# Kernel optimization log

Measured on AMD Instinct MI355X. Metric: run time of the kernel, lower is better.

The kernel has to match this reference:

```python
import jax, jax.numpy as jnp
import numpy as np

DIM = 1024
B, T = 4, 8192


def setup_inputs() -> dict:
    key = jax.random.key(0)
    ks = jax.random.split(key, 5)
    scale = 1.0 / np.sqrt(DIM)
    x = jax.random.normal(ks[0], (B, T, DIM), dtype=jnp.float32)
    w_in = jax.random.uniform(ks[1], (DIM, DIM), jnp.float32, -scale, scale)
    b_in = jax.random.uniform(ks[2], (DIM,), jnp.float32, -scale, scale)
    a = jnp.zeros((DIM,), jnp.float32)   # nn.Parameter(torch.zeros(dim))
    b = jnp.ones((DIM,), jnp.float32)    # nn.Parameter(torch.ones(dim))
    w_out = jax.random.uniform(ks[3], (DIM, DIM), jnp.float32, -scale, scale)
    b_out = jax.random.uniform(ks[4], (DIM,), jnp.float32, -scale, scale)
    return {"x": x, "w_in": w_in, "b_in": b_in, "a": a, "b": b,
            "w_out": w_out, "b_out": b_out}


def reference(x, w_in, b_in, a, b, w_out, b_out):
    # h = in_proj(x): [B, T, D]
    h = jnp.einsum('btd,ed->bte', x, w_in) + b_in
    A = jax.nn.sigmoid(a)  # [D], diagonal transition

    def step(state, h_t):
        state = A * state + b * h_t  # [B, D]
        return state, state

    init = jnp.zeros_like(h[:, 0])  # [B, D]
    _, ys = jax.lax.scan(step, init, jnp.swapaxes(h, 0, 1))  # ys: [T, B, D]
    y = jnp.swapaxes(ys, 0, 1)  # [B, T, D]
    return jnp.einsum('btd,ed->bte', y, w_out) + b_out
```

## Files before the change

### kernel.cpp

```cpp
#include <hip/hip_runtime.h>
#include <hip/hip_bf16.h>
#include <cstdint>

#define DIM 1024
#define BATCH 4
#define SEQ 8192
#define M_TOTAL (BATCH * SEQ)

#define CH 64
#define CL (SEQ / CH)

using bf16 = __hip_bfloat16;
typedef __attribute__((ext_vector_type(4))) float f32x4;
typedef __attribute__((ext_vector_type(8))) __bf16 bf16x8;

__global__ void f32_to_bf16_vec(const float* __restrict__ in,
                                bf16* __restrict__ out, long n4) {
    long i = blockIdx.x * (long)blockDim.x + threadIdx.x;
    if (i >= n4) return;
    const float4 v = ((const float4*)in)[i];
    __hip_bfloat162* o = (__hip_bfloat162*)(out + i * 4);
    o[0] = __float22bfloat162_rn(make_float2(v.x, v.y));
    o[1] = __float22bfloat162_rn(make_float2(v.z, v.w));
}

template <int OUT_MODE>
__global__ __launch_bounds__(256) void gemm_bt_kernel(
    const bf16* __restrict__ A, const bf16* __restrict__ B,
    const float* __restrict__ bias, void* __restrict__ C,
    int M, int N, int K) {
    __shared__ __align__(16) char lds[2 * 128 * 32 * 2];
    char* ldsA = lds;
    char* ldsB = lds + 128 * 32 * 2;

    const int tid  = threadIdx.x;
    const int wave = tid >> 6;
    const int lane = tid & 63;
    const int bm = blockIdx.x;
    const int bn = blockIdx.y;
    const int wm = (wave >> 1) * 64;
    const int wn = (wave & 1) * 64;

    f32x4 acc[4][4];
#pragma unroll
    for (int i = 0; i < 4; i++)
#pragma unroll
        for (int j = 0; j < 4; j++) acc[i][j] = (f32x4){0.f, 0.f, 0.f, 0.f};

    const long arow_base = (long)bm * 128;
    const long brow_base = (long)bn * 128;

    const int fr_row = lane & 15;
    const int fr_kb  = lane >> 4;

    for (int k0 = 0; k0 < K; k0 += 32) {
#pragma unroll
        for (int r = 0; r < 2; r++) {
            int c = tid + r * 256;
            int row = c >> 2, kc = c & 3;
            const bf16* ga = A + (arow_base + row) * K + k0 + kc * 8;
            const bf16* gb = B + (brow_base + row) * K + k0 + kc * 8;
            __builtin_amdgcn_global_load_lds(
                (const __attribute__((address_space(1))) void*)ga,
                (__attribute__((address_space(3))) void*)(ldsA + c * 16),
                16, 0, 0);
            __builtin_amdgcn_global_load_lds(
                (const __attribute__((address_space(1))) void*)gb,
                (__attribute__((address_space(3))) void*)(ldsB + c * 16),
                16, 0, 0);
        }
        __syncthreads();

        bf16x8 af[4], bfg[4];
#pragma unroll
        for (int i = 0; i < 4; i++) {
            int rowA = wm + i * 16 + fr_row;
            af[i] = *(const bf16x8*)(ldsA + rowA * 64 + fr_kb * 16);
        }
#pragma unroll
        for (int j = 0; j < 4; j++) {
            int rowB = wn + j * 16 + fr_row;
            bfg[j] = *(const bf16x8*)(ldsB + rowB * 64 + fr_kb * 16);
        }
#pragma unroll
        for (int i = 0; i < 4; i++)
#pragma unroll
            for (int j = 0; j < 4; j++)
                acc[i][j] = __builtin_amdgcn_mfma_f32_16x16x32_bf16(
                    af[i], bfg[j], acc[i][j], 0, 0, 0);
        __syncthreads();
    }

    const int crow = (lane >> 4) * 4;
    const int ccol = lane & 15;
#pragma unroll
    for (int i = 0; i < 4; i++) {
#pragma unroll
        for (int j = 0; j < 4; j++) {
            long mbase = (long)bm * 128 + wm + i * 16 + crow;
            int n = bn * 128 + wn + j * 16 + ccol;
            float bv = bias[n];
#pragma unroll
            for (int r = 0; r < 4; r++) {
                float v = acc[i][j][r] + bv;
                long idx = (mbase + r) * (long)N + n;
                if (OUT_MODE == 0)
                    ((bf16*)C)[idx] = __float2bfloat16(v);
                else
                    ((float*)C)[idx] = v;
            }
        }
    }
}

__global__ __launch_bounds__(1024) void scan_pass1(
    const bf16* __restrict__ h, const float* __restrict__ a,
    const float* __restrict__ bcoef, float* __restrict__ S) {
    const int d = threadIdx.x;
    const int blk = blockIdx.x;
    const int b = blk / CH, c = blk % CH;
    const float Ad = 1.f / (1.f + expf(-a[d]));
    const float bd = bcoef[d];
    float s = 0.f;
    const bf16* hp = h + ((long)b * SEQ + (long)c * CL) * DIM + d;
#pragma unroll 4
    for (int t = 0; t < CL; t++)
        s = Ad * s + bd * __bfloat162float(hp[(long)t * DIM]);
    S[((long)b * CH + c) * DIM + d] = s;
}

__global__ __launch_bounds__(1024) void scan_pass2(
    const float* __restrict__ S, const float* __restrict__ a,
    float* __restrict__ In) {
    const int d = threadIdx.x;
    const int b = blockIdx.x;
    const float Ad = 1.f / (1.f + expf(-a[d]));
    float Ap = Ad;
#pragma unroll
    for (int i = 0; i < 7; i++) Ap *= Ap;
    float carry = 0.f;
    for (int c = 0; c < CH; c++) {
        In[((long)b * CH + c) * DIM + d] = carry;
        carry = Ap * carry + S[((long)b * CH + c) * DIM + d];
    }
}

__global__ __launch_bounds__(1024) void scan_pass3(
    bf16* __restrict__ h, const float* __restrict__ a,
    const float* __restrict__ bcoef, const float* __restrict__ In) {
    const int d = threadIdx.x;
    const int blk = blockIdx.x;
    const int b = blk / CH, c = blk % CH;
    const float Ad = 1.f / (1.f + expf(-a[d]));
    const float bd = bcoef[d];
    float s = In[((long)b * CH + c) * DIM + d];
    bf16* hp = h + ((long)b * SEQ + (long)c * CL) * DIM + d;
#pragma unroll 4
    for (int t = 0; t < CL; t++) {
        s = Ad * s + bd * __bfloat162float(hp[(long)t * DIM]);
        hp[(long)t * DIM] = __float2bfloat16(s);
    }
}

extern "C" void kernel_launch(void* const* d_in, const int* in_sizes, int n_in,
                              void* d_out, int out_size, void* d_ws,
                              size_t ws_size, hipStream_t stream) {
    const float* x     = (const float*)d_in[0];
    const float* w_in  = (const float*)d_in[1];
    const float* b_in  = (const float*)d_in[2];
    const float* a     = (const float*)d_in[3];
    const float* bcoef = (const float*)d_in[4];
    const float* w_out = (const float*)d_in[5];
    const float* b_out = (const float*)d_in[6];
    float* out = (float*)d_out;

    char* ws = (char*)d_ws;
    bf16* xb  = (bf16*)ws;  ws += (size_t)M_TOTAL * DIM * 2;
    bf16* wib = (bf16*)ws;  ws += (size_t)DIM * DIM * 2;
    bf16* wob = (bf16*)ws;  ws += (size_t)DIM * DIM * 2;
    bf16* h   = (bf16*)ws;  ws += (size_t)M_TOTAL * DIM * 2;
    float* S  = (float*)ws; ws += (size_t)BATCH * CH * DIM * 4;
    float* In = (float*)ws; ws += (size_t)BATCH * CH * DIM * 4;

    {
        long n4 = (long)M_TOTAL * DIM / 4;
        f32_to_bf16_vec<<<(int)((n4 + 255) / 256), 256, 0, stream>>>(x, xb, n4);
        long w4 = (long)DIM * DIM / 4;
        f32_to_bf16_vec<<<(int)((w4 + 255) / 256), 256, 0, stream>>>(w_in, wib, w4);
        f32_to_bf16_vec<<<(int)((w4 + 255) / 256), 256, 0, stream>>>(w_out, wob, w4);
    }

    dim3 gg(M_TOTAL / 128, DIM / 128);

    gemm_bt_kernel<0><<<gg, 256, 0, stream>>>(xb, wib, b_in, h, M_TOTAL, DIM, DIM);

    scan_pass1<<<BATCH * CH, DIM, 0, stream>>>(h, a, bcoef, S);
    scan_pass2<<<BATCH, DIM, 0, stream>>>(S, a, In);
    scan_pass3<<<BATCH * CH, DIM, 0, stream>>>(h, a, bcoef, In);

    gemm_bt_kernel<1><<<gg, 256, 0, stream>>>(h, wob, b_out, out, M_TOTAL, DIM, DIM);
}
```

Before: 467.1 us.

## Fuse conversion kernels, widen GEMM K-tile with swizzled LDS, fold scan carry pass

Merges the three fp32-to-bf16 conversion launches into one kernel. The GEMM K-tile grows from 32 to 64 and uses an XOR-swizzled LDS layout to cut bank conflicts and halve the number of barriers per K. The grid is transposed so consecutive blocks share the same A rows. The separate carry-propagation scan pass is removed: each chunk block recomputes its incoming carry from the chunk sums, and the scan unroll factor is raised. This adds redundant per-block carry work and doubles LDS per block, which may lower occupancy.

Measured after the change: 448.8 us. -3.9%, faster.

```diff
diff --git a/kernel.cpp b/kernel.cpp
--- a/kernel.cpp
+++ b/kernel.cpp
@@ -14,12 +14,20 @@
 typedef __attribute__((ext_vector_type(4))) float f32x4;
 typedef __attribute__((ext_vector_type(8))) __bf16 bf16x8;
 
-__global__ void f32_to_bf16_vec(const float* __restrict__ in,
-                                bf16* __restrict__ out, long n4) {
+__global__ void convert_all(const float* __restrict__ x, bf16* __restrict__ xb,
+                            const float* __restrict__ w1, bf16* __restrict__ w1b,
+                            const float* __restrict__ w2, bf16* __restrict__ w2b,
+                            long n4x, long n4w) {
     long i = blockIdx.x * (long)blockDim.x + threadIdx.x;
-    if (i >= n4) return;
-    const float4 v = ((const float4*)in)[i];
-    __hip_bfloat162* o = (__hip_bfloat162*)(out + i * 4);
+    const float* in;
+    bf16* out;
+    long off;
+    if (i < n4x)              { in = x;  out = xb;  off = i; }
+    else if (i < n4x + n4w)   { in = w1; out = w1b; off = i - n4x; }
+    else if (i < n4x + 2*n4w) { in = w2; out = w2b; off = i - n4x - n4w; }
+    else return;
+    const float4 v = ((const float4*)in)[off];
+    __hip_bfloat162* o = (__hip_bfloat162*)(out + off * 4);
     o[0] = __float22bfloat162_rn(make_float2(v.x, v.y));
     o[1] = __float22bfloat162_rn(make_float2(v.z, v.w));
 }
@@ -29,15 +37,15 @@
     const bf16* __restrict__ A, const bf16* __restrict__ B,
     const float* __restrict__ bias, void* __restrict__ C,
     int M, int N, int K) {
-    __shared__ __align__(16) char lds[2 * 128 * 32 * 2];
+    __shared__ __align__(16) char lds[2 * 128 * 64 * 2];
     char* ldsA = lds;
-    char* ldsB = lds + 128 * 32 * 2;
+    char* ldsB = lds + 128 * 64 * 2;
 
     const int tid  = threadIdx.x;
     const int wave = tid >> 6;
     const int lane = tid & 63;
-    const int bm = blockIdx.x;
-    const int bn = blockIdx.y;
+    const int bn = blockIdx.x;
+    const int bm = blockIdx.y;
     const int wm = (wave >> 1) * 64;
     const int wn = (wave & 1) * 64;
 
@@ -53,13 +61,14 @@
     const int fr_row = lane & 15;
     const int fr_kb  = lane >> 4;
 
-    for (int k0 = 0; k0 < K; k0 += 32) {
-#pragma unroll
-        for (int r = 0; r < 2; r++) {
+    for (int k0 = 0; k0 < K; k0 += 64) {
+#pragma unroll
+        for (int r = 0; r < 4; r++) {
             int c = tid + r * 256;
-            int row = c >> 2, kc = c & 3;
-            const bf16* ga = A + (arow_base + row) * K + k0 + kc * 8;
-            const bf16* gb = B + (brow_base + row) * K + k0 + kc * 8;
+            int row = c >> 3;
+            int kc = (c & 7) ^ (row & 7);
+            const bf16* ga = A + (arow_base + row) * (long)K + k0 + kc * 8;
+            const bf16* gb = B + (brow_base + row) * (long)K + k0 + kc * 8;
             __builtin_amdgcn_global_load_lds(
                 (const __attribute__((address_space(1))) void*)ga,
                 (__attribute__((address_space(3))) void*)(ldsA + c * 16),
@@ -71,23 +80,30 @@
         }
         __syncthreads();
 
-        bf16x8 af[4], bfg[4];
-#pragma unroll
-        for (int i = 0; i < 4; i++) {
-            int rowA = wm + i * 16 + fr_row;
-            af[i] = *(const bf16x8*)(ldsA + rowA * 64 + fr_kb * 16);
+#pragma unroll
+        for (int ks = 0; ks < 2; ks++) {
+            bf16x8 af[4], bfg[4];
+#pragma unroll
+            for (int i = 0; i < 4; i++) {
+                int row = wm + i * 16 + fr_row;
+                int cc = ks * 4 + fr_kb;
+                int chunk = row * 8 + (cc ^ (row & 7));
+                af[i] = *(const bf16x8*)(ldsA + chunk * 16);
+            }
+#pragma unroll
+            for (int j = 0; j < 4; j++) {
+                int row = wn + j * 16 + fr_row;
+                int cc = ks * 4 + fr_kb;
+                int chunk = row * 8 + (cc ^ (row & 7));
+                bfg[j] = *(const bf16x8*)(ldsB + chunk * 16);
+            }
+#pragma unroll
+            for (int i = 0; i < 4; i++)
+#pragma unroll
+                for (int j = 0; j < 4; j++)
+                    acc[i][j] = __builtin_amdgcn_mfma_f32_16x16x32_bf16(
+                        af[i], bfg[j], acc[i][j], 0, 0, 0);
         }
-#pragma unroll
-        for (int j = 0; j < 4; j++) {
-            int rowB = wn + j * 16 + fr_row;
-            bfg[j] = *(const bf16x8*)(ldsB + rowB * 64 + fr_kb * 16);
-        }
-#pragma unroll
-        for (int i = 0; i < 4; i++)
-#pragma unroll
-            for (int j = 0; j < 4; j++)
-                acc[i][j] = __builtin_amdgcn_mfma_f32_16x16x32_bf16(
-                    af[i], bfg[j], acc[i][j], 0, 0, 0);
         __syncthreads();
     }
 
@@ -123,39 +139,40 @@
     const float bd = bcoef[d];
     float s = 0.f;
     const bf16* hp = h + ((long)b * SEQ + (long)c * CL) * DIM + d;
-#pragma unroll 4
+#pragma unroll 8
     for (int t = 0; t < CL; t++)
         s = Ad * s + bd * __bfloat162float(hp[(long)t * DIM]);
     S[((long)b * CH + c) * DIM + d] = s;
 }
 
-__global__ __launch_bounds__(1024) void scan_pass2(
-    const float* __restrict__ S, const float* __restrict__ a,
-    float* __restrict__ In) {
-    const int d = threadIdx.x;
-    const int b = blockIdx.x;
-    const float Ad = 1.f / (1.f + expf(-a[d]));
-    float Ap = Ad;
-#pragma unroll
-    for (int i = 0; i < 7; i++) Ap *= Ap;
-    float carry = 0.f;
-    for (int c = 0; c < CH; c++) {
-        In[((long)b * CH + c) * DIM + d] = carry;
-        carry = Ap * carry + S[((long)b * CH + c) * DIM + d];
-    }
-}
-
 __global__ __launch_bounds__(1024) void scan_pass3(
     bf16* __restrict__ h, const float* __restrict__ a,
-    const float* __restrict__ bcoef, const float* __restrict__ In) {
+    const float* __restrict__ bcoef, const float* __restrict__ S) {
     const int d = threadIdx.x;
     const int blk = blockIdx.x;
     const int b = blk / CH, c = blk % CH;
     const float Ad = 1.f / (1.f + expf(-a[d]));
     const float bd = bcoef[d];
-    float s = In[((long)b * CH + c) * DIM + d];
+    float Ap = Ad;
+#pragma unroll
+    for (int i = 0; i < 7; i++) Ap *= Ap;
+
+    float carry = 0.f;
+    const float* Sp = S + (long)b * CH * DIM + d;
+    for (int i0 = 0; i0 < c; i0 += 8) {
+        float sv[8];
+        int nn = (c - i0 < 8) ? (c - i0) : 8;
+#pragma unroll 8
+        for (int j = 0; j < 8; j++)
+            if (j < nn) sv[j] = Sp[(long)(i0 + j) * DIM];
+#pragma unroll 8
+        for (int j = 0; j < 8; j++)
+            if (j < nn) carry = Ap * carry + sv[j];
+    }
+
+    float s = carry;
     bf16* hp = h + ((long)b * SEQ + (long)c * CL) * DIM + d;
-#pragma unroll 4
+#pragma unroll 8
     for (int t = 0; t < CL; t++) {
         s = Ad * s + bd * __bfloat162float(hp[(long)t * DIM]);
         hp[(long)t * DIM] = __float2bfloat16(s);
@@ -180,23 +197,21 @@
     bf16* wob = (bf16*)ws;  ws += (size_t)DIM * DIM * 2;
     bf16* h   = (bf16*)ws;  ws += (size_t)M_TOTAL * DIM * 2;
     float* S  = (float*)ws; ws += (size_t)BATCH * CH * DIM * 4;
-    float* In = (float*)ws; ws += (size_t)BATCH * CH * DIM * 4;
 
     {
-        long n4 = (long)M_TOTAL * DIM / 4;
-        f32_to_bf16_vec<<<(int)((n4 + 255) / 256), 256, 0, stream>>>(x, xb, n4);
-        long w4 = (long)DIM * DIM / 4;
-        f32_to_bf16_vec<<<(int)((w4 + 255) / 256), 256, 0, stream>>>(w_in, wib, w4);
-        f32_to_bf16_vec<<<(int)((w4 + 255) / 256), 256, 0, stream>>>(w_out, wob, w4);
-    }
-
-    dim3 gg(M_TOTAL / 128, DIM / 128);
+        long n4x = (long)M_TOTAL * DIM / 4;
+        long n4w = (long)DIM * DIM / 4;
+        long total = n4x + 2 * n4w;
+        convert_all<<<(int)((total + 255) / 256), 256, 0, stream>>>(
+            x, xb, w_in, wib, w_out, wob, n4x, n4w);
+    }
+
+    dim3 gg(DIM / 128, M_TOTAL / 128);
 
     gemm_bt_kernel<0><<<gg, 256, 0, stream>>>(xb, wib, b_in, h, M_TOTAL, DIM, DIM);
 
     scan_pass1<<<BATCH * CH, DIM, 0, stream>>>(h, a, bcoef, S);
-    scan_pass2<<<BATCH, DIM, 0, stream>>>(S, a, In);
-    scan_pass3<<<BATCH * CH, DIM, 0, stream>>>(h, a, bcoef, In);
+    scan_pass3<<<BATCH * CH, DIM, 0, stream>>>(h, a, bcoef, S);
 
     gemm_bt_kernel<1><<<gg, 256, 0, stream>>>(h, wob, b_out, out, M_TOTAL, DIM, DIM);
 }
```
